# Kernel optimization log

Hardware: AMD Instinct MI355X
Metric: run time of the kernel (lower is better)

Reference implementation:

```python
import jax, jax.numpy as jnp
import numpy as np
from jax import lax

K = 3
STRIDE = 1
PAD = 1


def setup_inputs() -> dict:
    key = jax.random.key(0)
    k1, k2, k3 = jax.random.split(key, 3)
    x = jax.random.normal(k1, (4, 256, 64, 64), dtype=jnp.float32)
    # offset-conv weight: C_in=256 -> 2*K*K=18 offset channels
    w_off = jax.random.normal(k2, (18, 256, 3, 3), dtype=jnp.float32) * 0.01
    # deformable conv weight: C_in=256 -> C_out=256
    w_def = jax.random.normal(k3, (256, 256, 3, 3), dtype=jnp.float32) * 0.05
    return {"x": x, "w_off": w_off, "w_def": w_def}


def _deform_conv(x, offset, w_def):
    # x: [B,C,H,W]; offset: [B,2*K*K,Ho,Wo] torchvision layout (dy,dx interleaved)
    B, C, H, W = x.shape
    Ho, Wo = offset.shape[2], offset.shape[3]
    KK = K * K
    off = offset.reshape(B, KK, 2, Ho, Wo)
    ky, kx = jnp.meshgrid(jnp.arange(K), jnp.arange(K), indexing="ij")
    ky = ky.reshape(KK).astype(x.dtype)  # kernel tap row offsets
    kx = kx.reshape(KK).astype(x.dtype)
    base_y = (jnp.arange(Ho, dtype=x.dtype) * STRIDE - PAD)[None, :, None] + ky[:, None, None]  # [KK,Ho,1]
    base_x = (jnp.arange(Wo, dtype=x.dtype) * STRIDE - PAD)[None, None, :] + kx[:, None, None]  # [KK,1,Wo]
    py = off[:, :, 0] + base_y  # [B,KK,Ho,Wo]
    px = off[:, :, 1] + base_x

    def sample_one(img, py1, px1):
        # img: [C,H,W]; py1/px1: [KK,Ho,Wo]
        y0f = jnp.floor(py1)
        x0f = jnp.floor(px1)
        wy1 = py1 - y0f
        wx1 = px1 - x0f
        wy0 = 1.0 - wy1
        wx0 = 1.0 - wx1
        y0 = y0f.astype(jnp.int32)
        x0 = x0f.astype(jnp.int32)
        y1 = y0 + 1
        x1 = x0 + 1

        def gather(yi, xi):
            valid = (yi >= 0) & (yi < H) & (xi >= 0) & (xi < W)
            yc = jnp.clip(yi, 0, H - 1)
            xc = jnp.clip(xi, 0, W - 1)
            v = img[:, yc, xc]  # [C,KK,Ho,Wo]
            return v * valid[None].astype(img.dtype)

        out = (wy0 * wx0)[None] * gather(y0, x0)
        out = out + (wy0 * wx1)[None] * gather(y0, x1)
        out = out + (wy1 * wx0)[None] * gather(y1, x0)
        out = out + (wy1 * wx1)[None] * gather(y1, x1)
        return out  # [C,KK,Ho,Wo]

    sampled = jax.vmap(sample_one)(x, py, px)  # [B,C,KK,Ho,Wo]
    w = w_def.reshape(w_def.shape[0], C, KK)
    return jnp.einsum("bckhw,ock->bohw", sampled, w)


def reference(x, w_off, w_def):
    offset = lax.conv_general_dilated(
        x, w_off, window_strides=(STRIDE, STRIDE),
        padding=[(PAD, PAD), (PAD, PAD)],
        dimension_numbers=("NCHW", "OIHW", "NCHW"),
    )
    return _deform_conv(x, offset, w_def)
```

## Files before the change

### kernel.cpp

```cpp
#include <hip/hip_runtime.h>

typedef __attribute__((ext_vector_type(8))) short short8;
typedef __attribute__((ext_vector_type(4))) float f32x4;
typedef __attribute__((ext_vector_type(4))) unsigned int u32x4;
typedef unsigned short ushort_t;

constexpr int B   = 4;
constexpr int C   = 256;
constexpr int H   = 64;
constexpr int W   = 64;
constexpr int HW  = H * W;
constexpr int OCH = 256;
constexpr int KT  = 9 * C;
constexpr int NHS = KT / 32;

__device__ __forceinline__ ushort_t f2bf(float f) {
    unsigned u = __float_as_uint(f);
    u += 0x7FFF + ((u >> 16) & 1);
    return (ushort_t)(u >> 16);
}

__device__ __forceinline__ void block_sync_lds() {
    asm volatile("s_waitcnt lgkmcnt(0)" ::: "memory");
    __builtin_amdgcn_s_barrier();
    asm volatile("" ::: "memory");
}

__global__ __launch_bounds__(256) void prep_all(
    const float* __restrict__ x, const float* __restrict__ w_def,
    const float* __restrict__ w_off, ushort_t* __restrict__ xt01,
    ushort_t* __restrict__ xtD, ushort_t* __restrict__ wPack,
    ushort_t* __restrict__ wOffA)
{
    __shared__ float sT[64][65];
    int blk = blockIdx.x;
    if (blk < 1024) {
        int cg  = blk & 3;
        int y   = (blk >> 2) & 63;
        int b   = blk >> 8;
        int t   = threadIdx.x;
        int col = t & 63, r4 = t >> 6;

        const float* xp = x + (((size_t)b * C + cg * 64) * H + y) * W;
        #pragma unroll
        for (int i = 0; i < 16; ++i) {
            int cl = i * 4 + r4;
            sT[cl][col] = xp[(size_t)cl * HW + col];
        }
        __syncthreads();
        ushort_t* base = (b < 2) ? (xt01 + (size_t)b * HW * C)
                                 : (xtD + (size_t)(b - 2) * HW * C);
        ushort_t* op = base + ((size_t)y * W) * C + cg * 64;
        #pragma unroll
        for (int i = 0; i < 16; ++i) {
            int xl = i * 4 + r4;
            op[(size_t)xl * C + col] = f2bf(sT[col][xl]);
        }
    } else {
        int tid = (blk - 1024) * 256 + threadIdx.x;
        if (tid < NHS * 16 * 64) {
            int lane = tid & 63;
            int o = ((tid >> 6) & 15) * 16 + (lane & 15);
            int kbase = (tid >> 10) * 32 + (lane >> 4) * 8;
            union { ushort_t u[8]; short8 v; } pk;
            #pragma unroll
            for (int j = 0; j < 8; ++j) {
                int kidx = kbase + j;
                int c = kidx & 255, tap = kidx >> 8;
                pk.u[j] = f2bf(w_def[((size_t)o * C + c) * 9 + tap]);
            }
            *(short8*)(wPack + (size_t)tid * 8) = pk.v;
        } else {
            int t2 = tid - NHS * 16 * 64;
            int lane = t2 & 63;
            int o = ((t2 >> 6) & 1) * 16 + (lane & 15);
            int kbase = (t2 >> 7) * 32 + (lane >> 4) * 8;
            union { ushort_t u[8]; short8 v; } pk;
            #pragma unroll
            for (int j = 0; j < 8; ++j) {
                int kidx = kbase + j;
                int c = kidx & 255, tap = kidx >> 8;
                pk.u[j] = (o < 18) ? f2bf(w_off[((size_t)o * C + c) * 9 + tap]) : (ushort_t)0;
            }
            *(short8*)(wOffA + (size_t)t2 * 8) = pk.v;
        }
    }
}

__global__ __launch_bounds__(512, 2) void deform_pair(
    const ushort_t* __restrict__ xtB, const ushort_t* __restrict__ wOffA,
    const ushort_t* __restrict__ wPack, float* __restrict__ out, int pbase)
{
    __shared__ __align__(16) ushort_t sS[2][32][33][8];
    __shared__ float sOff[18][32];
    __shared__ float sPart[8][18][32];
    __shared__ int   sBase[2][128];
    __shared__ float sWgt[2][32][4];

    int orig = blockIdx.x;
    int r = ((orig & 7) << 5) | (orig >> 3);
    int bl = r >> 7, ho = (r >> 1) & 63, pxh = r & 1;
    int tid = threadIdx.x;
    int lane = tid & 63, wv = tid >> 6;
    int chunk = tid & 15, rq = (tid >> 4) & 31;

    const ushort_t* xtb = xtB + (size_t)bl * HW * C;
    int b = pbase + bl;

    {
        const short8* wA = (const short8*)wOffA;
        f32x4 pacc[2][2];
        #pragma unroll
        for (int i = 0; i < 2; ++i)
            #pragma unroll
            for (int j = 0; j < 2; ++j) pacc[i][j] = (f32x4){0.f, 0.f, 0.f, 0.f};

        #pragma unroll 1
        for (int i = 0; i < 9; ++i) {
            int ks = wv * 9 + i;
            int tap = ks >> 3, cs = ks & 7;
            int ky = tap / 3, kx = tap - ky * 3;
            int y  = ho - 1 + ky;
            int yc = min(max(y, 0), 63);
            bool yok = ((unsigned)y < 64u);
            short8 a0 = wA[(size_t)ks * 128 + lane];
            short8 a1 = wA[(size_t)ks * 128 + 64 + lane];
            #pragma unroll
            for (int pt = 0; pt < 2; ++pt) {
                int px = pxh * 32 + pt * 16 + (lane & 15);
                int xx = px - 1 + kx;
                bool ok = yok && ((unsigned)xx < 64u);
                unsigned msk = ok ? 0xffffffffu : 0u;
                int xc = min(max(xx, 0), 63);
                const ushort_t* srcb = xtb + (size_t)(yc * 64 + xc) * C
                                       + cs * 32 + (lane >> 4) * 8;
                union { u32x4 u; short8 s; } bv;
                bv.u = *(const u32x4*)srcb;
                bv.u[0] &= msk; bv.u[1] &= msk; bv.u[2] &= msk; bv.u[3] &= msk;
                pacc[0][pt] = __builtin_amdgcn_mfma_f32_16x16x32_bf16(a0, bv.s, pacc[0][pt], 0, 0, 0);
                pacc[1][pt] = __builtin_amdgcn_mfma_f32_16x16x32_bf16(a1, bv.s, pacc[1][pt], 0, 0, 0);
            }
        }
        #pragma unroll
        for (int gt = 0; gt < 2; ++gt) {
            #pragma unroll
            for (int pt = 0; pt < 2; ++pt) {
                #pragma unroll
                for (int j = 0; j < 4; ++j) {
                    int oc = gt * 16 + (lane >> 4) * 4 + j;
                    if (oc < 18)
                        sPart[wv][oc][pt * 16 + (lane & 15)] = pacc[gt][pt][j];
                }
            }
        }
    }
    __syncthreads();
    for (int idx = tid; idx < 18 * 32; idx += 512) {
        int oc = idx >> 5, q = idx & 31;
        float s = 0.f;
        #pragma unroll
        for (int g = 0; g < 8; ++g) s += sPart[g][oc][q];
        sOff[oc][q] = s;
    }
    __syncthreads();

    f32x4 acc2[2][2];
    #pragma unroll
    for (int i = 0; i < 2; ++i)
        #pragma unroll
        for (int j = 0; j < 2; ++j) acc2[i][j] = (f32x4){0.f, 0.f, 0.f, 0.f};

    auto computeBase = [&](int tap, int buf) {
        if (tid < 128) {
            int n = tid >> 5, q = tid & 31;
            int ky = tap / 3, kx = tap - ky * 3;
            float offy = sOff[2 * tap][q];
            float offx = sOff[2 * tap + 1][q];
            float py  = offy + (float)(ho - 1 + ky);
            float pxf = offx + (float)(pxh * 32 + q - 1 + kx);
            float y0f = floorf(py), x0f = floorf(pxf);
            float wy1 = py - y0f, wx1 = pxf - x0f;
            int y0 = (int)y0f, x0 = (int)x0f;
            int dy = n >> 1, dx = n & 1;
            int yy = y0 + dy, xx = x0 + dx;
            float wn = (dy ? wy1 : (1.f - wy1)) * (dx ? wx1 : (1.f - wx1));
            wn *= (((unsigned)yy < 64u) ? 1.f : 0.f) * (((unsigned)xx < 64u) ? 1.f : 0.f);
            int yc = min(max(yy, 0), 63), xc = min(max(xx, 0), 63);
            sBase[buf][tid] = (yc * 64 + xc) * C;
            sWgt[buf][q][n] = wn;
        }
    };

    auto loadBases = [&](int buf, int* rb) {
        #pragma unroll
        for (int n = 0; n < 4; ++n) rb[n] = sBase[buf][n * 32 + rq];
    };

    auto issueBoth = [&](const int* rb, u32x4* La, u32x4* Lb) {
        #pragma unroll
        for (int n = 0; n < 4; ++n) {
            const ushort_t* p0 = xtb + rb[n] + chunk * 8;
            La[n] = *(const u32x4*)p0;
            Lb[n] = *(const u32x4*)(p0 + 128);
        }
    };

    auto blendOne = [&](const u32x4* L, const float* w, int p, int slot) {
        unsigned pk[4];
        #pragma unroll
        for (int j = 0; j < 4; ++j) {
            float f0l = __uint_as_float(L[0][j] << 16);
            float f0h = __uint_as_float(L[0][j] & 0xffff0000u);
            float f1l = __uint_as_float(L[1][j] << 16);
            float f1h = __uint_as_float(L[1][j] & 0xffff0000u);
            float f2l = __uint_as_float(L[2][j] << 16);
            float f2h = __uint_as_float(L[2][j] & 0xffff0000u);
            float f3l = __uint_as_float(L[3][j] << 16);
            float f3h = __uint_as_float(L[3][j] & 0xffff0000u);
            float lo = fmaf(w[0], f0l, fmaf(w[1], f1l, fmaf(w[2], f2l, w[3] * f3l)));
            float hi = fmaf(w[0], f0h, fmaf(w[1], f1h, fmaf(w[2], f2h, w[3] * f3h)));
            asm("v_cvt_pk_bf16_f32 %0, %1, %2" : "=v"(pk[j]) : "v"(lo), "v"(hi));
        }
        u32x4 wvec = (u32x4){pk[0], pk[1], pk[2], pk[3]};
        *(u32x4*)&sS[p][slot][rq][0] = wvec;
    };

    int gt0 = wv * 2;
    const short8* wpB = (const short8*)wPack;

    auto loadA8 = [&](int ks4base, short8* A) {
        #pragma unroll
        for (int h = 0; h < 4; ++h) {
            size_t an = ((size_t)(ks4base + h) * 16 + gt0) * 64 + lane;
            A[2 * h]     = wpB[an];
            A[2 * h + 1] = wpB[an + 64];
        }
    };

    auto mfmaHalf = [&](const short8* A, int p, int half) {
        __builtin_amdgcn_s_setprio(1);
        #pragma unroll
        for (int h = 0; h < 4; ++h) {
            #pragma unroll
            for (int pt = 0; pt < 2; ++pt) {
                short8 bF = *(const short8*)&sS[p][half * 16 + h * 4 + (lane >> 4)][pt * 16 + (lane & 15)][0];
                acc2[0][pt] = __builtin_amdgcn_mfma_f32_16x16x32_bf16(A[2 * h],     bF, acc2[0][pt], 0, 0, 0);
                acc2[1][pt] = __builtin_amdgcn_mfma_f32_16x16x32_bf16(A[2 * h + 1], bF, acc2[1][pt], 0, 0, 0);
            }
        }
        __builtin_amdgcn_s_setprio(0);
    };

    u32x4 LA[4], LB[4];
    short8 A[8];

    computeBase(0, 0);
    block_sync_lds();
    {
        int rb0[4];
        loadBases(0, rb0);
        issueBoth(rb0, LA, LB);
    }

    int p = 0;
    #pragma unroll 1
    for (int tap = 0; tap < 9; ++tap) {
        float wcur[4];
        *(float4*)&wcur[0] = *(const float4*)&sWgt[tap & 1][rq][0];
        if (tap < 8) computeBase(tap + 1, (tap + 1) & 1);

        loadA8(tap * 8, A);
        blendOne(LA, wcur, p, chunk);
        blendOne(LB, wcur, p, 16 + chunk);
        block_sync_lds();

        int rb[4];
        if (tap < 8) { loadBases((tap + 1) & 1, rb); issueBoth(rb, LA, LB); }

        mfmaHalf(A, p, 0);
        loadA8(tap * 8 + 4, A);
        mfmaHalf(A, p, 1);
        p ^= 1;
    }

    #pragma unroll
    for (int ot = 0; ot < 2; ++ot) {
        int o = wv * 32 + ot * 16 + (lane >> 4) * 4;
        #pragma unroll
        for (int pt = 0; pt < 2; ++pt) {
            int pxx = pxh * 32 + pt * 16 + (lane & 15);
            #pragma unroll
            for (int j = 0; j < 4; ++j)
                out[(((size_t)b * OCH + (o + j)) * H + ho) * W + pxx] = acc2[ot][pt][j];
        }
    }
}

extern "C" void kernel_launch(void* const* d_in, const int* in_sizes, int n_in,
                              void* d_out, int out_size, void* d_ws, size_t ws_size,
                              hipStream_t stream)
{
    const float* x     = (const float*)d_in[0];
    const float* w_off = (const float*)d_in[1];
    const float* w_def = (const float*)d_in[2];
    float* out = (float*)d_out;

    ushort_t* xt01  = (ushort_t*)d_ws;
    ushort_t* wPack = xt01 + (size_t)2 * HW * C;
    ushort_t* wOffA = wPack + (size_t)NHS * 16 * 64 * 8;
    ushort_t* xtD   = (ushort_t*)d_out;

    prep_all<<<1348, 256, 0, stream>>>(x, w_def, w_off, xt01, xtD, wPack, wOffA);
    deform_pair<<<256, 512, 0, stream>>>(xtD, wOffA, wPack, out, 2);
    deform_pair<<<256, 512, 0, stream>>>(xt01, wOffA, wPack, out, 0);
}
```

Before: 64.78 us.

## Split output channels across two blocks to double grid size

Each block now computes only half of the output channels (selected by a new ohalf bit in the block index), and the grid doubles from 256 to 512 blocks per launch. Per-wave accumulators and A-fragment loads are halved, which reduces register pressure and MFMA work per block. The offset convolution and the bilinear sampling into LDS are now duplicated across the two channel halves. This trades redundant gather and offset work for higher CU occupancy.

```diff
diff --git a/kernel.cpp b/kernel.cpp
--- a/kernel.cpp
+++ b/kernel.cpp
@@ -98,8 +98,8 @@
     __shared__ float sWgt[2][32][4];
 
     int orig = blockIdx.x;
-    int r = ((orig & 7) << 5) | (orig >> 3);
-    int bl = r >> 7, ho = (r >> 1) & 63, pxh = r & 1;
+    int r = ((orig & 7) << 6) | (orig >> 3);
+    int bl = r >> 8, ho = (r >> 2) & 63, ohalf = (r >> 1) & 1, pxh = r & 1;
     int tid = threadIdx.x;
     int lane = tid & 63, wv = tid >> 6;
     int chunk = tid & 15, rq = (tid >> 4) & 31;
@@ -164,11 +164,9 @@
     }
     __syncthreads();
 
-    f32x4 acc2[2][2];
-    #pragma unroll
-    for (int i = 0; i < 2; ++i)
-        #pragma unroll
-        for (int j = 0; j < 2; ++j) acc2[i][j] = (f32x4){0.f, 0.f, 0.f, 0.f};
+    f32x4 acc2[2];
+    acc2[0] = (f32x4){0.f, 0.f, 0.f, 0.f};
+    acc2[1] = (f32x4){0.f, 0.f, 0.f, 0.f};
 
     auto computeBase = [&](int tap, int buf) {
         if (tid < 128) {
@@ -225,16 +223,13 @@
         *(u32x4*)&sS[p][slot][rq][0] = wvec;
     };
 
-    int gt0 = wv * 2;
+    int gt0 = ohalf * 8 + wv;
     const short8* wpB = (const short8*)wPack;
 
-    auto loadA8 = [&](int ks4base, short8* A) {
-        #pragma unroll
-        for (int h = 0; h < 4; ++h) {
-            size_t an = ((size_t)(ks4base + h) * 16 + gt0) * 64 + lane;
-            A[2 * h]     = wpB[an];
-            A[2 * h + 1] = wpB[an + 64];
-        }
+    auto loadA4 = [&](int ks4base, short8* A) {
+        #pragma unroll
+        for (int h = 0; h < 4; ++h)
+            A[h] = wpB[((size_t)(ks4base + h) * 16 + gt0) * 64 + lane];
     };
 
     auto mfmaHalf = [&](const short8* A, int p, int half) {
@@ -244,15 +239,14 @@
             #pragma unroll
             for (int pt = 0; pt < 2; ++pt) {
                 short8 bF = *(const short8*)&sS[p][half * 16 + h * 4 + (lane >> 4)][pt * 16 + (lane & 15)][0];
-                acc2[0][pt] = __builtin_amdgcn_mfma_f32_16x16x32_bf16(A[2 * h],     bF, acc2[0][pt], 0, 0, 0);
-                acc2[1][pt] = __builtin_amdgcn_mfma_f32_16x16x32_bf16(A[2 * h + 1], bF, acc2[1][pt], 0, 0, 0);
+                acc2[pt] = __builtin_amdgcn_mfma_f32_16x16x32_bf16(A[h], bF, acc2[pt], 0, 0, 0);
             }
         }
         __builtin_amdgcn_s_setprio(0);
     };
 
     u32x4 LA[4], LB[4];
-    short8 A[8];
+    short8 A[4];
 
     computeBase(0, 0);
     block_sync_lds();
@@ -269,7 +263,7 @@
         *(float4*)&wcur[0] = *(const float4*)&sWgt[tap & 1][rq][0];
         if (tap < 8) computeBase(tap + 1, (tap + 1) & 1);
 
-        loadA8(tap * 8, A);
+        loadA4(tap * 8, A);
         blendOne(LA, wcur, p, chunk);
         blendOne(LB, wcur, p, 16 + chunk);
         block_sync_lds();
@@ -278,20 +272,19 @@
         if (tap < 8) { loadBases((tap + 1) & 1, rb); issueBoth(rb, LA, LB); }
 
         mfmaHalf(A, p, 0);
-        loadA8(tap * 8 + 4, A);
+        loadA4(tap * 8 + 4, A);
         mfmaHalf(A, p, 1);
         p ^= 1;
     }
 
-    #pragma unroll
-    for (int ot = 0; ot < 2; ++ot) {
-        int o = wv * 32 + ot * 16 + (lane >> 4) * 4;
+    {
+        int o = gt0 * 16 + (lane >> 4) * 4;
         #pragma unroll
         for (int pt = 0; pt < 2; ++pt) {
             int pxx = pxh * 32 + pt * 16 + (lane & 15);
             #pragma unroll
             for (int j = 0; j < 4; ++j)
-                out[(((size_t)b * OCH + (o + j)) * H + ho) * W + pxx] = acc2[ot][pt][j];
+                out[(((size_t)b * OCH + (o + j)) * H + ho) * W + pxx] = acc2[pt][j];
         }
     }
 }
@@ -311,6 +304,6 @@
     ushort_t* xtD   = (ushort_t*)d_out;
 
     prep_all<<<1348, 256, 0, stream>>>(x, w_def, w_off, xt01, xtD, wPack, wOffA);
-    deform_pair<<<256, 512, 0, stream>>>(xtD, wOffA, wPack, out, 2);
-    deform_pair<<<256, 512, 0, stream>>>(xt01, wOffA, wPack, out, 0);
-}
+    deform_pair<<<512, 512, 0, stream>>>(xtD, wOffA, wPack, out, 2);
+    deform_pair<<<512, 512, 0, stream>>>(xt01, wOffA, wPack, out, 0);
+}
```

Result: slower. 84.35 us (+30.2%).
